# Kernel tuning notes

Hardware: AMD Instinct MI355X
Metric: run time of the kernel (lower is better)

## Reference

```python
import jax, jax.numpy as jnp
import numpy as np

E, H = 1024, 16
N, S, T = 2, 2048, 2048


def setup_inputs() -> dict:
    key = jax.random.key(0)
    ks = jax.random.split(key, 8)
    scale = 1.0 / np.sqrt(E)
    q = jax.random.normal(ks[0], (N, S, E), dtype=jnp.float32)
    k = jax.random.normal(ks[1], (N, T, E), dtype=jnp.float32)
    v = jax.random.normal(ks[2], (N, T, E), dtype=jnp.float32)
    pad_mask = jax.random.randint(ks[3], (N, 1, 1, T), 0, 2, dtype=jnp.int32)
    subsq_mask = jnp.tril(jnp.ones((S, T), dtype=jnp.int32))[None, None]
    Wq = jax.random.normal(ks[4], (E, E), dtype=jnp.float32) * scale
    Wk = jax.random.normal(ks[5], (E, E), dtype=jnp.float32) * scale
    Wv = jax.random.normal(ks[6], (E, E), dtype=jnp.float32) * scale
    bq = jnp.zeros((E,), dtype=jnp.float32)
    bk = jnp.zeros((E,), dtype=jnp.float32)
    bv = jnp.zeros((E,), dtype=jnp.float32)
    return {"query": q, "key": k, "value": v, "pad_mask": pad_mask,
            "subsq_mask": subsq_mask, "Wq": Wq, "bq": bq, "Wk": Wk,
            "bk": bk, "Wv": Wv, "bv": bv}


def reference(query, key, value, pad_mask, subsq_mask, Wq, bq, Wk, bk, Wv, bv):
    n, s, e = query.shape
    t = value.shape[1]
    d = e // H
    # Linear projections (torch Linear: x @ W^T + b), split into heads
    q = (query @ Wq.T + bq).reshape(n, s, H, d).transpose(0, 2, 1, 3)  # [N,H,S,D]
    k = (key @ Wk.T + bk).reshape(n, t, H, d).transpose(0, 2, 1, 3)    # [N,H,T,D]
    v = (value @ Wv.T + bv).reshape(n, t, H, d).transpose(0, 2, 1, 3)  # [N,H,T,D]
    att = jnp.einsum('bhsd,bhtd->bhst', q, k) / jnp.sqrt(jnp.float32(d))
    att = jnp.where(pad_mask == 0, jnp.float32(-1e9), att)
    att = jnp.where(subsq_mask == 0, jnp.float32(-1e9), att)
    prob = jax.nn.softmax(att, axis=-1)
    out = jnp.einsum('bhst,bhtd->bhsd', prob, v)  # [N,H,S,D]
    return out.transpose(0, 2, 1, 3).reshape(n, s, e)
```

## Files before the change

kernel.cpp:

```cpp
#include <hip/hip_runtime.h>

#define HEADS 16
#define DH    64
#define EMB   1024
#define NBAT  2
#define SEQ   2048
#define KDIM  1024
#define NROW  (NBAT * SEQ)

typedef __attribute__((ext_vector_type(8))) short short8;
typedef __attribute__((ext_vector_type(4))) short short4v;
typedef __attribute__((ext_vector_type(4))) float floatx4;
typedef unsigned short u16;
typedef unsigned int   u32;

__device__ __forceinline__ u16 f2bf(float x) {
    u32 u = __builtin_bit_cast(u32, x);
    u += 0x7fffu + ((u >> 16) & 1u);
    return (u16)(u >> 16);
}
__device__ __forceinline__ float bf2f(u16 v) {
    return __builtin_bit_cast(float, ((u32)v) << 16);
}

__device__ __forceinline__ void gll16(const u16* g, u16* l) {
    __builtin_amdgcn_global_load_lds((const __attribute__((address_space(1))) u32*)g,
                                     (__attribute__((address_space(3))) u32*)l, 16, 0, 0);
}

__global__ __launch_bounds__(256) void cvt_kernel(
    const float* __restrict__ q, const float* __restrict__ k, const float* __restrict__ v,
    const float* __restrict__ wq, const float* __restrict__ wk, const float* __restrict__ wv,
    u16* __restrict__ xb, u16* __restrict__ wb)
{
    const int z = blockIdx.y;
    const float* src; u16* dst; int n;
    if (z < 3) { src = (z == 0) ? q : (z == 1) ? k : v;     dst = xb + (size_t)z * 4194304;       n = 4194304; }
    else       { src = (z == 3) ? wq : (z == 4) ? wk : wv;  dst = wb + (size_t)(z - 3) * 1048576; n = 1048576; }
    for (int i = (blockIdx.x * 256 + threadIdx.x) * 8; i < n; i += 512 * 256 * 8) {
        float4 a = *(const float4*)(src + i);
        float4 b = *(const float4*)(src + i + 4);
        short8 o;
        o[0] = (short)f2bf(a.x); o[1] = (short)f2bf(a.y); o[2] = (short)f2bf(a.z); o[3] = (short)f2bf(a.w);
        o[4] = (short)f2bf(b.x); o[5] = (short)f2bf(b.y); o[6] = (short)f2bf(b.z); o[7] = (short)f2bf(b.w);
        *(short8*)(dst + i) = o;
    }
}

__global__ __launch_bounds__(256) void proj_kernel(
    const u16* __restrict__ xb, const u16* __restrict__ wb,
    const float* __restrict__ bq, const float* __restrict__ bk, const float* __restrict__ bv,
    u16* __restrict__ qh, u16* __restrict__ kh, u16* __restrict__ vt)
{
    const int z = blockIdx.z;
    const u16* A  = xb + (size_t)z * 4194304;
    const u16* B  = wb + (size_t)z * 1048576;
    const float* Bp = (z == 0) ? bq : (z == 1) ? bk : bv;
    u16* dst        = (z == 0) ? qh : (z == 1) ? kh : vt;

    const int m0 = blockIdx.y * 128;
    const int n0 = blockIdx.x * 128;
    const int tid  = threadIdx.x;
    const int wave = tid >> 6, lane = tid & 63;
    const int quad = lane >> 4, l15 = lane & 15;
    const int waveM = wave >> 1, waveN = wave & 1;

    __shared__ __align__(16) u16 As[128 * 64];
    __shared__ __align__(16) u16 Bs[128 * 64];

    floatx4 acc[4][4];
    for (int a = 0; a < 4; a++)
        for (int b = 0; b < 4; b++)
            acc[a][b] = floatx4{0.f, 0.f, 0.f, 0.f};

    const int lrow = lane >> 3, lcol = (lane & 7) * 8;

    for (int k0 = 0; k0 < KDIM; k0 += 64) {
        for (int j = 0; j < 4; j++) {
            int r8 = wave * 32 + j * 8;
            gll16(A + (size_t)(m0 + r8 + lrow) * KDIM + k0 + lcol, &As[r8 * 64]);
        }
        for (int j = 0; j < 4; j++) {
            int r8 = wave * 32 + j * 8;
            gll16(B + (size_t)(n0 + r8 + lrow) * KDIM + k0 + lcol, &Bs[r8 * 64]);
        }
        __syncthreads();

        for (int ks = 0; ks < 2; ks++) {
            short8 af[4], bfg[4];
            for (int mb = 0; mb < 4; mb++)
                af[mb]  = *(const short8*)&As[(waveM * 64 + mb * 16 + l15) * 64 + ks * 32 + quad * 8];
            for (int nb = 0; nb < 4; nb++)
                bfg[nb] = *(const short8*)&Bs[(waveN * 64 + nb * 16 + l15) * 64 + ks * 32 + quad * 8];
            for (int mb = 0; mb < 4; mb++)
                for (int nb = 0; nb < 4; nb++)
                    acc[mb][nb] = __builtin_amdgcn_mfma_f32_16x16x32_bf16(af[mb], bfg[nb], acc[mb][nb], 0, 0, 0);
        }
        __syncthreads();
    }

    const int row0 = m0 + waveM * 64;
    const int col0 = n0 + waveN * 64;
    const float scale = (z == 0) ? 0.125f : 1.0f;
    for (int nb = 0; nb < 4; nb++) {
        int col = col0 + nb * 16 + l15;
        float bias = Bp[col];
        int hh = col >> 6, dd = col & 63;
        for (int mb = 0; mb < 4; mb++) {
            for (int r = 0; r < 4; r++) {
                int row = row0 + mb * 16 + quad * 4 + r;
                int nn = row >> 11, ss = row & 2047;
                u16 o = f2bf((acc[mb][nb][r] + bias) * scale);
                if (z == 2)
                    dst[((size_t)(nn * HEADS + hh) * DH + dd) * SEQ + ss] = o;
                else
                    dst[((size_t)(nn * HEADS + hh) * SEQ + ss) * DH + dd] = o;
            }
        }
    }
}

__global__ __launch_bounds__(256) void vmean_kernel(const u16* __restrict__ vt,
                                                    float* __restrict__ vmean)
{
    const int row = blockIdx.x;
    const u16* p = vt + (size_t)row * SEQ;
    const int tid = threadIdx.x;
    float s = 0.f;
    for (int i = tid; i < SEQ; i += 256) s += bf2f(p[i]);
    __shared__ float red[256];
    red[tid] = s;
    __syncthreads();
    for (int st = 128; st > 0; st >>= 1) {
        if (tid < st) red[tid] += red[tid + st];
        __syncthreads();
    }
    if (tid == 0) vmean[row] = red[0] * (1.f / (float)SEQ);
}

__global__ __launch_bounds__(256) void attn_kernel(
    const u16* __restrict__ qh, const u16* __restrict__ kh, const u16* __restrict__ vt,
    const int* __restrict__ pad, const float* __restrict__ vmean,
    float* __restrict__ out)
{
    const int nh = blockIdx.y;
    const int n = nh >> 4, h = nh & 15;
    const int tid  = threadIdx.x;
    const int wave = tid >> 6, lane = tid & 63;
    const int quad = lane >> 4, l15 = lane & 15;

    __shared__ __align__(16) u16 Ks[64 * 72];
    __shared__ __align__(16) u16 Vs[64 * 72];
    __shared__ __align__(16) u16 Ps[64 * 72];
    __shared__ int pads[SEQ];

    for (int i = tid; i < SEQ; i += 256) pads[i] = pad[n * SEQ + i];

    const u16* qbase = qh + (size_t)nh * SEQ * DH;
    const u16* kbase = kh + (size_t)nh * SEQ * DH;
    const u16* vbase = vt + (size_t)nh * DH * SEQ;

    short8 ones;
    for (int i = 0; i < 8; i++) ones[i] = (short)0x3F80;

    float vm[4];
    for (int nd = 0; nd < 4; nd++) vm[nd] = vmean[nh * DH + nd * 16 + l15];

    const int ldrow = (lane >> 3), ldcol = (lane & 7) * 8;

    for (int half = 0; half < 2; half++) {
        const int sb = (half == 0) ? blockIdx.x : (31 - blockIdx.x);
        const int s0 = sb * 64;
        const int nt = sb + 1;
        const int srow = s0 + wave * 16 + l15;

        short8 qf[2];
        for (int ks = 0; ks < 2; ks++)
            qf[ks] = *(const short8*)(qbase + (size_t)srow * DH + ks * 32 + quad * 8);

        floatx4 oacc[4];
        for (int nd = 0; nd < 4; nd++) oacc[nd] = floatx4{0.f, 0.f, 0.f, 0.f};
        floatx4 lacc = floatx4{0.f, 0.f, 0.f, 0.f};

        short8 rK[2], rV[2];
        {
            const int t0 = 0;
            for (int i = 0; i < 2; i++) {
                int idx = i * 256 + tid, row = idx >> 3, c = (idx & 7) * 8;
                rK[i] = *(const short8*)(kbase + (size_t)(t0 + row) * DH + c);
                rV[i] = *(const short8*)(vbase + (size_t)row * SEQ + t0 + c);
            }
        }

        for (int tb = 0; tb < nt; tb++) {
            __syncthreads();
            for (int i = 0; i < 2; i++) {
                int idx = i * 256 + tid, row = idx >> 3, c = (idx & 7) * 8;
                *(short8*)&Ks[row * 72 + c] = rK[i];
                *(short8*)&Vs[row * 72 + c] = rV[i];
            }
            __syncthreads();

            if (tb + 1 < nt) {
                const int t0n = (tb + 1) * 64;
                for (int i = 0; i < 2; i++) {
                    int idx = i * 256 + tid, row = idx >> 3, c = (idx & 7) * 8;
                    rK[i] = *(const short8*)(kbase + (size_t)(t0n + row) * DH + c);
                    rV[i] = *(const short8*)(vbase + (size_t)row * SEQ + t0n + c);
                }
            }

            const int t0 = tb * 64;

            floatx4 sc[4];
            for (int nb = 0; nb < 4; nb++) sc[nb] = floatx4{0.f, 0.f, 0.f, 0.f};
            for (int ks = 0; ks < 2; ks++) {
                for (int nb = 0; nb < 4; nb++) {
                    short8 kf = *(const short8*)&Ks[(nb * 16 + l15) * 72 + ks * 32 + quad * 8];
                    sc[nb] = __builtin_amdgcn_mfma_f32_16x16x32_bf16(kf, qf[ks], sc[nb], 0, 0, 0);
                }
            }

            for (int nb = 0; nb < 4; nb++) {
                short4v pk;
                for (int r = 0; r < 4; r++) {
                    int t = t0 + nb * 16 + quad * 4 + r;
                    float p = (pads[t] != 0 && t <= srow) ? __expf(sc[nb][r]) : 0.f;
                    pk[r] = (short)f2bf(p);
                }
                *(short4v*)&Ps[(wave * 16 + l15) * 72 + nb * 16 + quad * 4] = pk;
            }
            asm volatile("s_waitcnt lgkmcnt(0)" ::: "memory");

            for (int ks = 0; ks < 2; ks++) {
                short8 pa = *(const short8*)&Ps[(wave * 16 + l15) * 72 + ks * 32 + quad * 8];
                for (int nd = 0; nd < 4; nd++) {
                    short8 vb = *(const short8*)&Vs[(nd * 16 + l15) * 72 + ks * 32 + quad * 8];
                    oacc[nd] = __builtin_amdgcn_mfma_f32_16x16x32_bf16(pa, vb, oacc[nd], 0, 0, 0);
                }
                lacc = __builtin_amdgcn_mfma_f32_16x16x32_bf16(pa, ones, lacc, 0, 0, 0);
            }
        }

        for (int r = 0; r < 4; r++) {
            float l = lacc[r];
            int s = s0 + wave * 16 + quad * 4 + r;
            float* orow = out + (size_t)(n * SEQ + s) * EMB + h * DH;
            if (l > 0.f) {
                float inv = 1.f / l;
                for (int nd = 0; nd < 4; nd++) orow[nd * 16 + l15] = oacc[nd][r] * inv;
            } else {
                for (int nd = 0; nd < 4; nd++) orow[nd * 16 + l15] = vm[nd];
            }
        }
    }
}

extern "C" void kernel_launch(void* const* d_in, const int* in_sizes, int n_in,
                              void* d_out, int out_size, void* d_ws, size_t ws_size,
                              hipStream_t stream)
{
    const float* qin = (const float*)d_in[0];
    const float* kin = (const float*)d_in[1];
    const float* vin = (const float*)d_in[2];
    const int*   pad = (const int*)d_in[3];
    const float* Wq = (const float*)d_in[5];
    const float* bq = (const float*)d_in[6];
    const float* Wk = (const float*)d_in[7];
    const float* bk = (const float*)d_in[8];
    const float* Wv = (const float*)d_in[9];
    const float* bv = (const float*)d_in[10];
    float* out = (float*)d_out;

    const size_t per = (size_t)NBAT * HEADS * SEQ * DH;
    u16* qh = (u16*)d_ws;
    u16* kh = qh + per;
    u16* vt = kh + per;
    float* vmean = (float*)(vt + per);
    u16* xb = (u16*)(vmean + 2048);
    u16* wb = xb + 3 * per;

    cvt_kernel<<<dim3(512, 6), 256, 0, stream>>>(qin, kin, vin, Wq, Wk, Wv, xb, wb);
    proj_kernel<<<dim3(EMB / 128, NROW / 128, 3), 256, 0, stream>>>(
        xb, wb, bq, bk, bv, qh, kh, vt);
    vmean_kernel<<<dim3(NBAT * HEADS * DH), 256, 0, stream>>>(vt, vmean);
    attn_kernel<<<dim3(16, NBAT * HEADS), 256, 0, stream>>>(qh, kh, vt, pad, vmean, out);
}
```

Baseline: 242.8 us.

## Remap blocks for XCD locality, double-buffer K/V, bitmask pad, coalesce V-transpose store

The projection and attention kernels now use a flattened 1D grid, remapped so blocks sharing the same weight rows or head land on the same XCD, which should improve L2 reuse. The attention loop double-buffers the K/V shared tiles, cutting one barrier per tile. The pad mask is packed into 64-bit ballot words, and the causal comparison runs only on the diagonal tile. The transposed V projection output is staged through shared memory so it can be written with coalesced 16-byte stores instead of scattered 2-byte ones. In exchange there is more shared memory per block and extra barriers in the V epilogue.

After: 230.9 us. 4.9% less time.

```diff
diff --git a/kernel.cpp b/kernel.cpp
--- a/kernel.cpp
+++ b/kernel.cpp
@@ -13,6 +13,7 @@
 typedef __attribute__((ext_vector_type(4))) float floatx4;
 typedef unsigned short u16;
 typedef unsigned int   u32;
+typedef unsigned long long u64;
 
 __device__ __forceinline__ u16 f2bf(float x) {
     u32 u = __builtin_bit_cast(u32, x);
@@ -52,21 +53,27 @@
     const float* __restrict__ bq, const float* __restrict__ bk, const float* __restrict__ bv,
     u16* __restrict__ qh, u16* __restrict__ kh, u16* __restrict__ vt)
 {
-    const int z = blockIdx.z;
+    const int f = blockIdx.x;
+    const int xcd = f & 7, jj = f >> 3;
+    const int g  = xcd * 12 + (jj >> 3);
+    const int nx = jj & 7;
+    const int z  = g >> 5, y = g & 31;
+
     const u16* A  = xb + (size_t)z * 4194304;
     const u16* B  = wb + (size_t)z * 1048576;
     const float* Bp = (z == 0) ? bq : (z == 1) ? bk : bv;
     u16* dst        = (z == 0) ? qh : (z == 1) ? kh : vt;
 
-    const int m0 = blockIdx.y * 128;
-    const int n0 = blockIdx.x * 128;
+    const int m0 = y * 128;
+    const int n0 = nx * 128;
     const int tid  = threadIdx.x;
     const int wave = tid >> 6, lane = tid & 63;
     const int quad = lane >> 4, l15 = lane & 15;
     const int waveM = wave >> 1, waveN = wave & 1;
 
-    __shared__ __align__(16) u16 As[128 * 64];
-    __shared__ __align__(16) u16 Bs[128 * 64];
+    __shared__ __align__(16) u16 smem[2 * 128 * 64];
+    u16* As = smem;
+    u16* Bs = smem + 128 * 64;
 
     floatx4 acc[4][4];
     for (int a = 0; a < 4; a++)
@@ -99,23 +106,48 @@
         __syncthreads();
     }
 
-    const int row0 = m0 + waveM * 64;
-    const int col0 = n0 + waveN * 64;
-    const float scale = (z == 0) ? 0.125f : 1.0f;
-    for (int nb = 0; nb < 4; nb++) {
-        int col = col0 + nb * 16 + l15;
-        float bias = Bp[col];
-        int hh = col >> 6, dd = col & 63;
-        for (int mb = 0; mb < 4; mb++) {
-            for (int r = 0; r < 4; r++) {
-                int row = row0 + mb * 16 + quad * 4 + r;
-                int nn = row >> 11, ss = row & 2047;
-                u16 o = f2bf((acc[mb][nb][r] + bias) * scale);
-                if (z == 2)
-                    dst[((size_t)(nn * HEADS + hh) * DH + dd) * SEQ + ss] = o;
-                else
-                    dst[((size_t)(nn * HEADS + hh) * SEQ + ss) * DH + dd] = o;
-            }
+    if (z != 2) {
+        const int row0 = m0 + waveM * 64;
+        const int col0 = n0 + waveN * 64;
+        const float scale = (z == 0) ? 0.125f : 1.0f;
+        for (int nb = 0; nb < 4; nb++) {
+            int col = col0 + nb * 16 + l15;
+            float bias = Bp[col];
+            int hh = col >> 6, dd = col & 63;
+            for (int mb = 0; mb < 4; mb++) {
+                for (int r = 0; r < 4; r++) {
+                    int row = row0 + mb * 16 + quad * 4 + r;
+                    int nn = row >> 11, ss = row & 2047;
+                    dst[((size_t)(nn * HEADS + hh) * SEQ + ss) * DH + dd] =
+                        f2bf((acc[mb][nb][r] + bias) * scale);
+                }
+            }
+        }
+    } else {
+        const int nn  = m0 >> 11;
+        const int ss0 = m0 & 2047;
+        for (int p = 0; p < 2; p++) {
+            if (waveN == p) {
+                for (int nb = 0; nb < 4; nb++) {
+                    int col_l = nb * 16 + l15;
+                    float bias = Bp[n0 + p * 64 + col_l];
+                    for (int mb = 0; mb < 4; mb++) {
+                        short4v pk;
+                        for (int r = 0; r < 4; r++)
+                            pk[r] = (short)f2bf(acc[mb][nb][r] + bias);
+                        *(short4v*)&smem[col_l * 136 + waveM * 64 + mb * 16 + quad * 4] = pk;
+                    }
+                }
+            }
+            __syncthreads();
+            const int hh = (n0 >> 6) + p;
+            u16* drow = dst + ((size_t)(nn * HEADS + hh) * DH) * SEQ + ss0;
+            for (int c2 = tid; c2 < 1024; c2 += 256) {
+                int dl = c2 >> 4, tc = (c2 & 15) * 8;
+                short8 vv = *(const short8*)&smem[dl * 136 + tc];
+                *(short8*)(drow + (size_t)dl * SEQ + tc) = vv;
+            }
+            __syncthreads();
         }
     }
 }
@@ -143,18 +175,28 @@
     const int* __restrict__ pad, const float* __restrict__ vmean,
     float* __restrict__ out)
 {
-    const int nh = blockIdx.y;
+    const int f = blockIdx.x;
+    const int xcd = f & 7, jj = f >> 3;
+    const int nh = xcd * 4 + (jj >> 4);
+    const int pr = jj & 15;
     const int n = nh >> 4, h = nh & 15;
     const int tid  = threadIdx.x;
     const int wave = tid >> 6, lane = tid & 63;
     const int quad = lane >> 4, l15 = lane & 15;
 
-    __shared__ __align__(16) u16 Ks[64 * 72];
-    __shared__ __align__(16) u16 Vs[64 * 72];
+    __shared__ __align__(16) u16 Ks[2][64 * 72];
+    __shared__ __align__(16) u16 Vs[2][64 * 72];
     __shared__ __align__(16) u16 Ps[64 * 72];
-    __shared__ int pads[SEQ];
-
-    for (int i = tid; i < SEQ; i += 256) pads[i] = pad[n * SEQ + i];
+    __shared__ u64 padb[32];
+
+    {
+        const int* pp = pad + n * SEQ;
+        for (int i = 0; i < 8; i++) {
+            int seg = wave * 8 + i;
+            u64 m = __ballot(pp[seg * 64 + lane] != 0);
+            if (lane == 0) padb[seg] = m;
+        }
+    }
 
     const u16* qbase = qh + (size_t)nh * SEQ * DH;
     const u16* kbase = kh + (size_t)nh * SEQ * DH;
@@ -162,14 +204,11 @@
 
     short8 ones;
     for (int i = 0; i < 8; i++) ones[i] = (short)0x3F80;
-
     float vm[4];
     for (int nd = 0; nd < 4; nd++) vm[nd] = vmean[nh * DH + nd * 16 + l15];
 
-    const int ldrow = (lane >> 3), ldcol = (lane & 7) * 8;
-
     for (int half = 0; half < 2; half++) {
-        const int sb = (half == 0) ? blockIdx.x : (31 - blockIdx.x);
+        const int sb = half ? (31 - pr) : pr;
         const int s0 = sb * 64;
         const int nt = sb + 1;
         const int srow = s0 + wave * 16 + l15;
@@ -178,29 +217,25 @@
         for (int ks = 0; ks < 2; ks++)
             qf[ks] = *(const short8*)(qbase + (size_t)srow * DH + ks * 32 + quad * 8);
 
-        floatx4 oacc[4];
+        floatx4 oacc[4], lacc;
         for (int nd = 0; nd < 4; nd++) oacc[nd] = floatx4{0.f, 0.f, 0.f, 0.f};
-        floatx4 lacc = floatx4{0.f, 0.f, 0.f, 0.f};
+        lacc = floatx4{0.f, 0.f, 0.f, 0.f};
 
         short8 rK[2], rV[2];
-        {
-            const int t0 = 0;
+        for (int i = 0; i < 2; i++) {
+            int idx = i * 256 + tid, row = idx >> 3, c = (idx & 7) * 8;
+            rK[i] = *(const short8*)(kbase + (size_t)row * DH + c);
+            rV[i] = *(const short8*)(vbase + (size_t)row * SEQ + c);
+        }
+        __syncthreads();
+
+        for (int tb = 0; tb < nt; tb++) {
+            const int cur = tb & 1;
             for (int i = 0; i < 2; i++) {
                 int idx = i * 256 + tid, row = idx >> 3, c = (idx & 7) * 8;
-                rK[i] = *(const short8*)(kbase + (size_t)(t0 + row) * DH + c);
-                rV[i] = *(const short8*)(vbase + (size_t)row * SEQ + t0 + c);
-            }
-        }
-
-        for (int tb = 0; tb < nt; tb++) {
-            __syncthreads();
-            for (int i = 0; i < 2; i++) {
-                int idx = i * 256 + tid, row = idx >> 3, c = (idx & 7) * 8;
-                *(short8*)&Ks[row * 72 + c] = rK[i];
-                *(short8*)&Vs[row * 72 + c] = rV[i];
-            }
-            __syncthreads();
-
+                *(short8*)&Ks[cur][row * 72 + c] = rK[i];
+                *(short8*)&Vs[cur][row * 72 + c] = rV[i];
+            }
             if (tb + 1 < nt) {
                 const int t0n = (tb + 1) * 64;
                 for (int i = 0; i < 2; i++) {
@@ -209,23 +244,27 @@
                     rV[i] = *(const short8*)(vbase + (size_t)row * SEQ + t0n + c);
                 }
             }
+            __syncthreads();
 
             const int t0 = tb * 64;
+            const u64 w = padb[t0 >> 6];
+            const bool diag = (tb == sb);
 
             floatx4 sc[4];
             for (int nb = 0; nb < 4; nb++) sc[nb] = floatx4{0.f, 0.f, 0.f, 0.f};
-            for (int ks = 0; ks < 2; ks++) {
+            for (int ks = 0; ks < 2; ks++)
                 for (int nb = 0; nb < 4; nb++) {
-                    short8 kf = *(const short8*)&Ks[(nb * 16 + l15) * 72 + ks * 32 + quad * 8];
+                    short8 kf = *(const short8*)&Ks[cur][(nb * 16 + l15) * 72 + ks * 32 + quad * 8];
                     sc[nb] = __builtin_amdgcn_mfma_f32_16x16x32_bf16(kf, qf[ks], sc[nb], 0, 0, 0);
                 }
-            }
 
             for (int nb = 0; nb < 4; nb++) {
                 short4v pk;
                 for (int r = 0; r < 4; r++) {
-                    int t = t0 + nb * 16 + quad * 4 + r;
-                    float p = (pads[t] != 0 && t <= srow) ? __expf(sc[nb][r]) : 0.f;
+                    int sh = nb * 16 + quad * 4 + r;
+                    bool ok = ((w >> sh) & 1ull) != 0;
+                    if (diag) ok = ok && (t0 + sh <= srow);
+                    float p = ok ? __expf(sc[nb][r]) : 0.f;
                     pk[r] = (short)f2bf(p);
                 }
                 *(short4v*)&Ps[(wave * 16 + l15) * 72 + nb * 16 + quad * 4] = pk;
@@ -235,7 +274,7 @@
             for (int ks = 0; ks < 2; ks++) {
                 short8 pa = *(const short8*)&Ps[(wave * 16 + l15) * 72 + ks * 32 + quad * 8];
                 for (int nd = 0; nd < 4; nd++) {
-                    short8 vb = *(const short8*)&Vs[(nd * 16 + l15) * 72 + ks * 32 + quad * 8];
+                    short8 vb = *(const short8*)&Vs[cur][(nd * 16 + l15) * 72 + ks * 32 + quad * 8];
                     oacc[nd] = __builtin_amdgcn_mfma_f32_16x16x32_bf16(pa, vb, oacc[nd], 0, 0, 0);
                 }
                 lacc = __builtin_amdgcn_mfma_f32_16x16x32_bf16(pa, ones, lacc, 0, 0, 0);
@@ -281,8 +320,7 @@
     u16* wb = xb + 3 * per;
 
     cvt_kernel<<<dim3(512, 6), 256, 0, stream>>>(qin, kin, vin, Wq, Wk, Wv, xb, wb);
-    proj_kernel<<<dim3(EMB / 128, NROW / 128, 3), 256, 0, stream>>>(
-        xb, wb, bq, bk, bv, qh, kh, vt);
+    proj_kernel<<<dim3(768), 256, 0, stream>>>(xb, wb, bq, bk, bv, qh, kh, vt);
     vmean_kernel<<<dim3(NBAT * HEADS * DH), 256, 0, stream>>>(vt, vmean);
-    attn_kernel<<<dim3(16, NBAT * HEADS), 256, 0, stream>>>(qh, kh, vt, pad, vmean, out);
-}
+    attn_kernel<<<dim3(512), 256, 0, stream>>>(qh, kh, vt, pad, vmean, out);
+}
```
